# Kernel tuning notes

Measured on AMD Instinct MI355X. Metric: run time of the kernel, lower is better.

The kernel has to match this reference:

```python
import jax, jax.numpy as jnp
import numpy as np

def setup_inputs() -> dict:
    key = jax.random.key(0)
    k0, k1, k2, k3 = jax.random.split(key, 4)
    B, L, D, E, Dg = 2, 2048, 2048, 8, 256  # Dg = D // E
    x = jax.random.normal(k0, (B, L, D), dtype=jnp.float32)
    Wg = jax.random.normal(k1, (E, D), dtype=jnp.float32) * 0.02     # gate: Linear(D, E)
    Wd = jax.random.normal(k2, (E, Dg, D), dtype=jnp.float32) * 0.02  # down: Linear(D, Dg) per expert
    Wu = jax.random.normal(k3, (E, D, Dg), dtype=jnp.float32) * 0.02  # up:   Linear(Dg, D) per expert
    return {"x": x, "Wg": Wg, "Wd": Wd, "Wu": Wu, "k": 2}

def reference(x, Wg, Wd, Wu, k):
    B, L, D = x.shape
    E = Wg.shape[0]
    T = B * L
    xf = x.reshape(T, D)
    # gate scores: sigmoid(x @ Wg^T), then top-k gate values G and expert indices I
    S = jax.nn.sigmoid(xf @ Wg.T)            # [T, E]
    G, I = jax.lax.top_k(S, k)               # [T, k], [T, k]
    # combine weights per token per expert (zero for unselected experts);
    # equivalent to the original's one_hot + per-expert gather/scatter-add.
    w = jnp.zeros((T, E), x.dtype).at[jnp.arange(T)[:, None], I].add(G)  # [T, E]
    # down: sum_e w[t,e] * (Wd[e] @ x[t])
    down = jnp.einsum('te,egd,td->tg', w, Wd, xf)   # [T, Dg]
    # inner model is identity
    # up: sum_e w[t,e] * (Wu[e] @ down[t])
    up = jnp.einsum('te,edg,tg->td', w, Wu, down)   # [T, D]
    return up.reshape(B, L, D)
```

## Files before the change

### kernel.cpp

```cpp
#include <hip/hip_runtime.h>
#include <hip/hip_bf16.h>
#include <stdint.h>

#define T_TOK 4096
#define DIM   2048
#define NEXP  8
#define DG    256
#define TOPK  2

#define BM 128
#define BN 128
#define BK 32
#define NROWS  (T_TOK*TOPK + NEXP*BM)
#define NBLK_M (NROWS/BM)
#define KSPLIT 4

typedef __attribute__((ext_vector_type(8))) short short8;
typedef __attribute__((ext_vector_type(4))) float f32x4;

static __device__ __forceinline__ short f2bf(float f) {
    union { float f; uint32_t u; } v{f};
    uint32_t r = v.u + 0x7fffu + ((v.u >> 16) & 1u);
    return (short)(r >> 16);
}
static __device__ __forceinline__ float b2f(short s) {
    union { uint32_t u; float f; } v{((uint32_t)(unsigned short)s) << 16};
    return v.f;
}
static __device__ __forceinline__ short8 pack8(float4 a, float4 b) {
    short8 o;
    o[0] = f2bf(a.x); o[1] = f2bf(a.y); o[2] = f2bf(a.z); o[3] = f2bf(a.w);
    o[4] = f2bf(b.x); o[5] = f2bf(b.y); o[6] = f2bf(b.z); o[7] = f2bf(b.w);
    return o;
}

#define GLD16(g, l) \
    __builtin_amdgcn_global_load_lds((const __attribute__((address_space(1))) void*)(g), \
                                     (__attribute__((address_space(3))) void*)(l), 16, 0, 0)

__global__ __launch_bounds__(256) void gate_kernel(const float* __restrict__ x,
                                                   const float* __restrict__ Wg,
                                                   int* __restrict__ gidx,
                                                   float* __restrict__ gval,
                                                   short* __restrict__ x_bf)
{
    int token = blockIdx.x * 4 + (threadIdx.x >> 6);
    int lane  = threadIdx.x & 63;
    const float4* xr = (const float4*)(x + (size_t)token * DIM);

    float4 xv[8];
#pragma unroll
    for (int i = 0; i < 8; i++) xv[i] = xr[lane + 64 * i];

    short4* xb = (short4*)(x_bf + (size_t)token * DIM);
#pragma unroll
    for (int i = 0; i < 8; i++) {
        short4 o;
        o.x = f2bf(xv[i].x); o.y = f2bf(xv[i].y);
        o.z = f2bf(xv[i].z); o.w = f2bf(xv[i].w);
        xb[lane + 64 * i] = o;
    }

    float acc[NEXP];
#pragma unroll
    for (int e = 0; e < NEXP; e++) {
        const float4* wr = (const float4*)(Wg + e * DIM);
        float a = 0.0f;
#pragma unroll
        for (int i = 0; i < 8; i++) {
            float4 w = wr[lane + 64 * i];
            a += xv[i].x * w.x + xv[i].y * w.y + xv[i].z * w.z + xv[i].w * w.w;
        }
        acc[e] = a;
    }

#pragma unroll
    for (int m = 1; m < 64; m <<= 1) {
#pragma unroll
        for (int e = 0; e < NEXP; e++) acc[e] += __shfl_xor(acc[e], m, 64);
    }

    if (lane == 0) {
        float sg[NEXP];
#pragma unroll
        for (int e = 0; e < NEXP; e++) sg[e] = 1.0f / (1.0f + expf(-acc[e]));
        int i0 = 0;
#pragma unroll
        for (int e = 1; e < NEXP; e++) if (sg[e] > sg[i0]) i0 = e;
        int i1 = (i0 == 0) ? 1 : 0;
#pragma unroll
        for (int e = 0; e < NEXP; e++) if (e != i0 && e != i1 && sg[e] > sg[i1]) i1 = e;
        gidx[2 * token + 0] = i0;
        gidx[2 * token + 1] = i1;
        gval[2 * token + 0] = sg[i0];
        gval[2 * token + 1] = sg[i1];
    }
}

__global__ __launch_bounds__(1024) void bucket_kernel(const int* __restrict__ gidx,
                                                      int* __restrict__ rowtok,
                                                      int* __restrict__ rowpos,
                                                      int* __restrict__ seg_off)
{
    __shared__ int cnt[NEXP];
    __shared__ int cur[NEXP];
    int tid = threadIdx.x;
    if (tid < NEXP) cnt[tid] = 0;
    __syncthreads();

    for (int t = tid; t < T_TOK; t += 1024) {
        atomicAdd(&cnt[gidx[2 * t + 0]], 1);
        atomicAdd(&cnt[gidx[2 * t + 1]], 1);
    }
    __syncthreads();

    if (tid == 0) {
        int o = 0;
        for (int e = 0; e < NEXP; e++) {
            seg_off[e] = o;
            cur[e] = o;
            o += ((cnt[e] + BM - 1) / BM) * BM;
        }
        seg_off[NEXP] = o;
    }
    __syncthreads();

    for (int r = tid; r < NROWS; r += 1024) rowtok[r] = -1;
    __syncthreads();

    for (int t = tid; t < T_TOK; t += 1024) {
        for (int s = 0; s < TOPK; s++) {
            int e = gidx[2 * t + s];
            int p = atomicAdd(&cur[e], 1);
            rowtok[p] = t;
            rowpos[2 * t + s] = p;
        }
    }
}

template<int K, int KC, int Ntot, bool PART>
__global__ __launch_bounds__(256) void gemm_kernel(const short* __restrict__ A,
                                                   const float* __restrict__ Bf,
                                                   const int* __restrict__ rowtok,
                                                   const int* __restrict__ seg_off,
                                                   short* __restrict__ Cbf,
                                                   float* __restrict__ Cf32)
{
    __shared__ short As[BM][BK];
    __shared__ short Bs[BN][BK];

    int row0 = blockIdx.x * BM;
    if (row0 >= seg_off[NEXP]) return;
    int e = 0;
    while (row0 >= seg_off[e + 1]) ++e;
    int n0 = blockIdx.y * BN;
    int kb = blockIdx.z;
    int k_start = kb * KC;

    int tid = threadIdx.x;
    int w = tid >> 6, l = tid & 63;

    int r = l >> 2, c = l & 3;
    int gch = c ^ ((r >> 1) & 3);
    int ar0 = w * 16 + r, ar1 = 64 + w * 16 + r;
    int ta0 = rowtok[row0 + ar0]; if (ta0 < 0) ta0 = 0;
    int ta1 = rowtok[row0 + ar1]; if (ta1 < 0) ta1 = 0;
    const short* ag0 = A + (size_t)ta0 * K + k_start + gch * 8;
    const short* ag1 = A + (size_t)ta1 * K + k_start + gch * 8;
    auto ldsA0 = (__attribute__((address_space(3))) void*)&As[w * 16][0];
    auto ldsA1 = (__attribute__((address_space(3))) void*)&As[64 + w * 16][0];

    int bn = tid >> 1, h = tid & 1;
    const float4* bg = (const float4*)(Bf + (size_t)e * Ntot * K
                                          + (size_t)(n0 + bn) * K + k_start + h * 16);
    int sw = (bn >> 1) & 3;
    short* bs0 = &Bs[bn][((2 * h + 0) ^ sw) * 8];
    short* bs1 = &Bs[bn][((2 * h + 1) ^ sw) * 8];

    int mlane = l & 15, q = l >> 4;
    int rA = (q ^ ((mlane >> 1) & 3)) * 8;
    int wm = w >> 1, wn = w & 1;
    const short* pA = &As[wm * 64 + mlane][0] + rA;
    const short* pB = &Bs[wn * 64 + mlane][0] + rA;

    f32x4 acc[4][4] = {};

    float4 br0 = bg[0], br1 = bg[1], br2 = bg[2], br3 = bg[3];
    bg += 8;

    constexpr int NS = KC / BK;
    for (int t = 0; t < NS; ++t) {
        GLD16(ag0, ldsA0);
        GLD16(ag1, ldsA1);
        ag0 += BK; ag1 += BK;

        *(short8*)bs0 = pack8(br0, br1);
        *(short8*)bs1 = pack8(br2, br3);
        if (t + 1 < NS) { br0 = bg[0]; br1 = bg[1]; br2 = bg[2]; br3 = bg[3]; bg += 8; }
        __syncthreads();

        short8 a[4], b[4];
#pragma unroll
        for (int i = 0; i < 4; i++) a[i] = *(const short8*)(pA + i * 16 * BK);
#pragma unroll
        for (int j = 0; j < 4; j++) b[j] = *(const short8*)(pB + j * 16 * BK);

#pragma unroll
        for (int i = 0; i < 4; i++)
#pragma unroll
            for (int j = 0; j < 4; j++)
                acc[i][j] = __builtin_amdgcn_mfma_f32_16x16x32_bf16(a[i], b[j], acc[i][j], 0, 0, 0);
        __syncthreads();
    }

#pragma unroll
    for (int i = 0; i < 4; i++) {
        int rbase = row0 + wm * 64 + i * 16 + q * 4;
#pragma unroll
        for (int j = 0; j < 4; j++) {
            int col = n0 + wn * 64 + j * 16 + mlane;
#pragma unroll
            for (int rr = 0; rr < 4; rr++) {
                if (PART)
                    Cf32[((size_t)kb * NROWS + (rbase + rr)) * Ntot + col] = acc[i][j][rr];
                else
                    Cbf[(size_t)(rbase + rr) * Ntot + col] = f2bf(acc[i][j][rr]);
            }
        }
    }
}

__global__ __launch_bounds__(256) void combine1_kernel(const float* __restrict__ P,
                                                       const int* __restrict__ rowpos,
                                                       const float* __restrict__ gval,
                                                       short* __restrict__ dt)
{
    int t = blockIdx.x * 4 + (threadIdx.x >> 6);
    int d = threadIdx.x & 63;
    int   p0 = rowpos[2 * t], p1 = rowpos[2 * t + 1];
    float g0 = gval[2 * t],   g1 = gval[2 * t + 1];
    const float4* P4 = (const float4*)P;
    const size_t plane = (size_t)NROWS * DG / 4;

    float4 s0 = {0, 0, 0, 0}, s1 = {0, 0, 0, 0};
#pragma unroll
    for (int kb = 0; kb < KSPLIT; kb++) {
        float4 a = P4[kb * plane + (size_t)p0 * (DG / 4) + d];
        float4 b = P4[kb * plane + (size_t)p1 * (DG / 4) + d];
        s0.x += a.x; s0.y += a.y; s0.z += a.z; s0.w += a.w;
        s1.x += b.x; s1.y += b.y; s1.z += b.z; s1.w += b.w;
    }
    short4 o;
    o.x = f2bf(g0 * s0.x + g1 * s1.x);
    o.y = f2bf(g0 * s0.y + g1 * s1.y);
    o.z = f2bf(g0 * s0.z + g1 * s1.z);
    o.w = f2bf(g0 * s0.w + g1 * s1.w);
    ((short4*)(dt + (size_t)t * DG))[d] = o;
}

__global__ __launch_bounds__(256) void combine2_kernel(const short* __restrict__ ur,
                                                       const int* __restrict__ rowpos,
                                                       const float* __restrict__ gval,
                                                       float* __restrict__ out)
{
    int i = blockIdx.x * 256 + threadIdx.x;
    int t = i >> 9;
    int c = (i & 511) * 4;
    int   p0 = rowpos[2 * t], p1 = rowpos[2 * t + 1];
    float g0 = gval[2 * t],   g1 = gval[2 * t + 1];
    short4 u0 = *(const short4*)&ur[(size_t)p0 * DIM + c];
    short4 u1 = *(const short4*)&ur[(size_t)p1 * DIM + c];
    float4 o;
    o.x = g0 * b2f(u0.x) + g1 * b2f(u1.x);
    o.y = g0 * b2f(u0.y) + g1 * b2f(u1.y);
    o.z = g0 * b2f(u0.z) + g1 * b2f(u1.z);
    o.w = g0 * b2f(u0.w) + g1 * b2f(u1.w);
    *(float4*)&out[(size_t)t * DIM + c] = o;
}

extern "C" void kernel_launch(void* const* d_in, const int* in_sizes, int n_in,
                              void* d_out, int out_size, void* d_ws, size_t ws_size,
                              hipStream_t stream) {
    const float* x  = (const float*)d_in[0];
    const float* Wg = (const float*)d_in[1];
    const float* Wd = (const float*)d_in[2];
    const float* Wu = (const float*)d_in[3];
    float* out = (float*)d_out;

    char* p = (char*)d_ws;
    int*   gidx    = (int*)(p + 0);
    float* gval    = (float*)(p + 32768);
    int*   rowtok  = (int*)(p + 65536);
    int*   rowpos  = (int*)(p + 102400);
    int*   seg_off = (int*)(p + 135168);
    short* x_bf    = (short*)(p + 135424);
    float* dr_part = (float*)(p + 16912640);
    short* dt_bf   = (short*)(p + 54661376);
    short* ur_bf   = (short*)(p + 56758528);

    gate_kernel<<<T_TOK / 4, 256, 0, stream>>>(x, Wg, gidx, gval, x_bf);
    bucket_kernel<<<1, 1024, 0, stream>>>(gidx, rowtok, rowpos, seg_off);

    gemm_kernel<DIM, DIM / KSPLIT, DG, true>
        <<<dim3(NBLK_M, DG / BN, KSPLIT), 256, 0, stream>>>(
            x_bf, Wd, rowtok, seg_off, nullptr, dr_part);
    combine1_kernel<<<T_TOK / 4, 256, 0, stream>>>(dr_part, rowpos, gval, dt_bf);

    gemm_kernel<DG, DG, DIM, false>
        <<<dim3(NBLK_M, DIM / BN, 1), 256, 0, stream>>>(
            dt_bf, Wu, rowtok, seg_off, ur_bf, nullptr);
    combine2_kernel<<<T_TOK * DIM / 4 / 256, 256, 0, stream>>>(ur_bf, rowpos, gval, out);
}
```

Baseline: 210.0 us.

## Pre-convert expert weights to bf16, double-buffer GEMM via async LDS loads

The gate kernel now also converts Wd and Wu to bf16 into workspace. The GEMM then loads both A and B tiles with global_load_lds into double-buffered shared memory, replacing the in-loop fp32→bf16 pack, and drops one barrier per K step. Split-K partials are stored as bf16 instead of fp32 with KSPLIT raised to 8, and the epilogue writes short4 vectors by swapping the MFMA operands. This trades extra weight-conversion traffic on every call and lower partial-sum precision for cheaper GEMM inner loops and less partial-buffer traffic.

```diff
diff --git a/kernel.cpp b/kernel.cpp
--- a/kernel.cpp
+++ b/kernel.cpp
@@ -13,7 +13,7 @@
 #define BK 32
 #define NROWS  (T_TOK*TOPK + NEXP*BM)
 #define NBLK_M (NROWS/BM)
-#define KSPLIT 4
+#define KSPLIT 8
 
 typedef __attribute__((ext_vector_type(8))) short short8;
 typedef __attribute__((ext_vector_type(4))) float f32x4;
@@ -27,22 +27,20 @@
     union { uint32_t u; float f; } v{((uint32_t)(unsigned short)s) << 16};
     return v.f;
 }
-static __device__ __forceinline__ short8 pack8(float4 a, float4 b) {
-    short8 o;
-    o[0] = f2bf(a.x); o[1] = f2bf(a.y); o[2] = f2bf(a.z); o[3] = f2bf(a.w);
-    o[4] = f2bf(b.x); o[5] = f2bf(b.y); o[6] = f2bf(b.z); o[7] = f2bf(b.w);
-    return o;
-}
-
+
+#define LDSP(p) ((__attribute__((address_space(3))) void*)(p))
 #define GLD16(g, l) \
-    __builtin_amdgcn_global_load_lds((const __attribute__((address_space(1))) void*)(g), \
-                                     (__attribute__((address_space(3))) void*)(l), 16, 0, 0)
+    __builtin_amdgcn_global_load_lds((const __attribute__((address_space(1))) void*)(g), LDSP(l), 16, 0, 0)
 
 __global__ __launch_bounds__(256) void gate_kernel(const float* __restrict__ x,
                                                    const float* __restrict__ Wg,
+                                                   const float* __restrict__ Wd,
+                                                   const float* __restrict__ Wu,
                                                    int* __restrict__ gidx,
                                                    float* __restrict__ gval,
-                                                   short* __restrict__ x_bf)
+                                                   short* __restrict__ x_bf,
+                                                   short* __restrict__ Wd_bf,
+                                                   short* __restrict__ Wu_bf)
 {
     int token = blockIdx.x * 4 + (threadIdx.x >> 6);
     int lane  = threadIdx.x & 63;
@@ -59,6 +57,20 @@
         o.x = f2bf(xv[i].x); o.y = f2bf(xv[i].y);
         o.z = f2bf(xv[i].z); o.w = f2bf(xv[i].w);
         xb[lane + 64 * i] = o;
+    }
+
+    int wi = blockIdx.x * 256 + threadIdx.x;
+#pragma unroll
+    for (int ii = 0; ii < 4; ii++) {
+        int j = wi + ii * 262144;
+        float4 v = ((const float4*)Wd)[j];
+        short4 o;
+        o.x = f2bf(v.x); o.y = f2bf(v.y); o.z = f2bf(v.z); o.w = f2bf(v.w);
+        ((short4*)Wd_bf)[j] = o;
+        float4 u = ((const float4*)Wu)[j];
+        short4 p;
+        p.x = f2bf(u.x); p.y = f2bf(u.y); p.z = f2bf(u.z); p.w = f2bf(u.w);
+        ((short4*)Wu_bf)[j] = p;
     }
 
     float acc[NEXP];
@@ -138,16 +150,15 @@
     }
 }
 
-template<int K, int KC, int Ntot, bool PART>
+template<int K, int KC, int Ntot>
 __global__ __launch_bounds__(256) void gemm_kernel(const short* __restrict__ A,
-                                                   const float* __restrict__ Bf,
+                                                   const short* __restrict__ B,
                                                    const int* __restrict__ rowtok,
                                                    const int* __restrict__ seg_off,
-                                                   short* __restrict__ Cbf,
-                                                   float* __restrict__ Cf32)
-{
-    __shared__ short As[BM][BK];
-    __shared__ short Bs[BN][BK];
+                                                   short* __restrict__ C)
+{
+    __shared__ short As[2][BM][BK];
+    __shared__ short Bs[2][BN][BK];
 
     int row0 = blockIdx.x * BM;
     if (row0 >= seg_off[NEXP]) return;
@@ -155,7 +166,7 @@
     while (row0 >= seg_off[e + 1]) ++e;
     int n0 = blockIdx.y * BN;
     int kb = blockIdx.z;
-    int k_start = kb * KC;
+    int ks = kb * KC;
 
     int tid = threadIdx.x;
     int w = tid >> 6, l = tid & 63;
@@ -165,72 +176,65 @@
     int ar0 = w * 16 + r, ar1 = 64 + w * 16 + r;
     int ta0 = rowtok[row0 + ar0]; if (ta0 < 0) ta0 = 0;
     int ta1 = rowtok[row0 + ar1]; if (ta1 < 0) ta1 = 0;
-    const short* ag0 = A + (size_t)ta0 * K + k_start + gch * 8;
-    const short* ag1 = A + (size_t)ta1 * K + k_start + gch * 8;
-    auto ldsA0 = (__attribute__((address_space(3))) void*)&As[w * 16][0];
-    auto ldsA1 = (__attribute__((address_space(3))) void*)&As[64 + w * 16][0];
-
-    int bn = tid >> 1, h = tid & 1;
-    const float4* bg = (const float4*)(Bf + (size_t)e * Ntot * K
-                                          + (size_t)(n0 + bn) * K + k_start + h * 16);
-    int sw = (bn >> 1) & 3;
-    short* bs0 = &Bs[bn][((2 * h + 0) ^ sw) * 8];
-    short* bs1 = &Bs[bn][((2 * h + 1) ^ sw) * 8];
+    const short* ag0 = A + (size_t)ta0 * K + ks + gch * 8;
+    const short* ag1 = A + (size_t)ta1 * K + ks + gch * 8;
+    const short* bb  = B + (size_t)e * Ntot * K + (size_t)n0 * K + ks + gch * 8;
+    const short* bg0 = bb + (size_t)ar0 * K;
+    const short* bg1 = bb + (size_t)ar1 * K;
 
     int mlane = l & 15, q = l >> 4;
     int rA = (q ^ ((mlane >> 1) & 3)) * 8;
     int wm = w >> 1, wn = w & 1;
-    const short* pA = &As[wm * 64 + mlane][0] + rA;
-    const short* pB = &Bs[wn * 64 + mlane][0] + rA;
 
     f32x4 acc[4][4] = {};
 
-    float4 br0 = bg[0], br1 = bg[1], br2 = bg[2], br3 = bg[3];
-    bg += 8;
-
     constexpr int NS = KC / BK;
+    GLD16(ag0, &As[0][w * 16][0]);
+    GLD16(ag1, &As[0][64 + w * 16][0]);
+    GLD16(bg0, &Bs[0][w * 16][0]);
+    GLD16(bg1, &Bs[0][64 + w * 16][0]);
+
     for (int t = 0; t < NS; ++t) {
-        GLD16(ag0, ldsA0);
-        GLD16(ag1, ldsA1);
-        ag0 += BK; ag1 += BK;
-
-        *(short8*)bs0 = pack8(br0, br1);
-        *(short8*)bs1 = pack8(br2, br3);
-        if (t + 1 < NS) { br0 = bg[0]; br1 = bg[1]; br2 = bg[2]; br3 = bg[3]; bg += 8; }
         __syncthreads();
-
+        if (t + 1 < NS) {
+            int nb = (t + 1) & 1;
+            int ko = (t + 1) * BK;
+            GLD16(ag0 + ko, &As[nb][w * 16][0]);
+            GLD16(ag1 + ko, &As[nb][64 + w * 16][0]);
+            GLD16(bg0 + ko, &Bs[nb][w * 16][0]);
+            GLD16(bg1 + ko, &Bs[nb][64 + w * 16][0]);
+        }
+        int cb = t & 1;
+        const short* pa = &As[cb][wm * 64 + mlane][0] + rA;
+        const short* pb = &Bs[cb][wn * 64 + mlane][0] + rA;
         short8 a[4], b[4];
 #pragma unroll
-        for (int i = 0; i < 4; i++) a[i] = *(const short8*)(pA + i * 16 * BK);
-#pragma unroll
-        for (int j = 0; j < 4; j++) b[j] = *(const short8*)(pB + j * 16 * BK);
+        for (int i = 0; i < 4; i++) a[i] = *(const short8*)(pa + i * 16 * BK);
+#pragma unroll
+        for (int j = 0; j < 4; j++) b[j] = *(const short8*)(pb + j * 16 * BK);
 
 #pragma unroll
         for (int i = 0; i < 4; i++)
 #pragma unroll
             for (int j = 0; j < 4; j++)
-                acc[i][j] = __builtin_amdgcn_mfma_f32_16x16x32_bf16(a[i], b[j], acc[i][j], 0, 0, 0);
-        __syncthreads();
+                acc[i][j] = __builtin_amdgcn_mfma_f32_16x16x32_bf16(b[j], a[i], acc[i][j], 0, 0, 0);
     }
 
 #pragma unroll
     for (int i = 0; i < 4; i++) {
-        int rbase = row0 + wm * 64 + i * 16 + q * 4;
+        size_t grow = (size_t)kb * NROWS + row0 + wm * 64 + i * 16 + mlane;
+        short* crow = C + grow * Ntot + n0 + wn * 64 + q * 4;
 #pragma unroll
         for (int j = 0; j < 4; j++) {
-            int col = n0 + wn * 64 + j * 16 + mlane;
-#pragma unroll
-            for (int rr = 0; rr < 4; rr++) {
-                if (PART)
-                    Cf32[((size_t)kb * NROWS + (rbase + rr)) * Ntot + col] = acc[i][j][rr];
-                else
-                    Cbf[(size_t)(rbase + rr) * Ntot + col] = f2bf(acc[i][j][rr]);
-            }
-        }
-    }
-}
-
-__global__ __launch_bounds__(256) void combine1_kernel(const float* __restrict__ P,
+            short4 v;
+            v.x = f2bf(acc[i][j][0]); v.y = f2bf(acc[i][j][1]);
+            v.z = f2bf(acc[i][j][2]); v.w = f2bf(acc[i][j][3]);
+            *(short4*)(crow + j * 16) = v;
+        }
+    }
+}
+
+__global__ __launch_bounds__(256) void combine1_kernel(const short* __restrict__ P,
                                                        const int* __restrict__ rowpos,
                                                        const float* __restrict__ gval,
                                                        short* __restrict__ dt)
@@ -239,22 +243,21 @@
     int d = threadIdx.x & 63;
     int   p0 = rowpos[2 * t], p1 = rowpos[2 * t + 1];
     float g0 = gval[2 * t],   g1 = gval[2 * t + 1];
-    const float4* P4 = (const float4*)P;
+    const short4* P4 = (const short4*)P;
     const size_t plane = (size_t)NROWS * DG / 4;
 
-    float4 s0 = {0, 0, 0, 0}, s1 = {0, 0, 0, 0};
+    float s0 = 0, s1 = 0, s2 = 0, s3 = 0;
 #pragma unroll
     for (int kb = 0; kb < KSPLIT; kb++) {
-        float4 a = P4[kb * plane + (size_t)p0 * (DG / 4) + d];
-        float4 b = P4[kb * plane + (size_t)p1 * (DG / 4) + d];
-        s0.x += a.x; s0.y += a.y; s0.z += a.z; s0.w += a.w;
-        s1.x += b.x; s1.y += b.y; s1.z += b.z; s1.w += b.w;
+        short4 a = P4[kb * plane + (size_t)p0 * (DG / 4) + d];
+        short4 b = P4[kb * plane + (size_t)p1 * (DG / 4) + d];
+        s0 += g0 * b2f(a.x) + g1 * b2f(b.x);
+        s1 += g0 * b2f(a.y) + g1 * b2f(b.y);
+        s2 += g0 * b2f(a.z) + g1 * b2f(b.z);
+        s3 += g0 * b2f(a.w) + g1 * b2f(b.w);
     }
     short4 o;
-    o.x = f2bf(g0 * s0.x + g1 * s1.x);
-    o.y = f2bf(g0 * s0.y + g1 * s1.y);
-    o.z = f2bf(g0 * s0.z + g1 * s1.z);
-    o.w = f2bf(g0 * s0.w + g1 * s1.w);
+    o.x = f2bf(s0); o.y = f2bf(s1); o.z = f2bf(s2); o.w = f2bf(s3);
     ((short4*)(dt + (size_t)t * DG))[d] = o;
 }
 
@@ -294,20 +297,20 @@
     int*   rowpos  = (int*)(p + 102400);
     int*   seg_off = (int*)(p + 135168);
     short* x_bf    = (short*)(p + 135424);
-    float* dr_part = (float*)(p + 16912640);
-    short* dt_bf   = (short*)(p + 54661376);
-    short* ur_bf   = (short*)(p + 56758528);
-
-    gate_kernel<<<T_TOK / 4, 256, 0, stream>>>(x, Wg, gidx, gval, x_bf);
+    short* Wd_bf   = (short*)(p + 16912640);
+    short* Wu_bf   = (short*)(p + 25301248);
+    short* P       = (short*)(p + 33689856);
+    short* dt_bf   = (short*)(p + 71438592);
+    short* ur_bf   = (short*)(p + 73535744);
+
+    gate_kernel<<<T_TOK / 4, 256, 0, stream>>>(x, Wg, Wd, Wu, gidx, gval, x_bf, Wd_bf, Wu_bf);
     bucket_kernel<<<1, 1024, 0, stream>>>(gidx, rowtok, rowpos, seg_off);
 
-    gemm_kernel<DIM, DIM / KSPLIT, DG, true>
-        <<<dim3(NBLK_M, DG / BN, KSPLIT), 256, 0, stream>>>(
-            x_bf, Wd, rowtok, seg_off, nullptr, dr_part);
-    combine1_kernel<<<T_TOK / 4, 256, 0, stream>>>(dr_part, rowpos, gval, dt_bf);
-
-    gemm_kernel<DG, DG, DIM, false>
-        <<<dim3(NBLK_M, DIM / BN, 1), 256, 0, stream>>>(
-            dt_bf, Wu, rowtok, seg_off, ur_bf, nullptr);
+    gemm_kernel<DIM, DIM / KSPLIT, DG>
+        <<<dim3(NBLK_M, DG / BN, KSPLIT), 256, 0, stream>>>(x_bf, Wd_bf, rowtok, seg_off, P);
+    combine1_kernel<<<T_TOK / 4, 256, 0, stream>>>(P, rowpos, gval, dt_bf);
+
+    gemm_kernel<DG, DG, DIM>
+        <<<dim3(NBLK_M, DIM / BN, 1), 256, 0, stream>>>(dt_bf, Wu_bf, rowtok, seg_off, ur_bf);
     combine2_kernel<<<T_TOK * DIM / 4 / 256, 256, 0, stream>>>(ur_bf, rowpos, gval, out);
 }
```

New measurement: 201.8 us. -3.9%, faster.
